# Kernel tuning notes

Measured on AMD Instinct MI355X. Metric: run time of the kernel, lower is better.

Reference implementation:

```python
import jax, jax.numpy as jnp
import numpy as np

# Module config (matches init_kwargs); num_heads must be 1 for the original
# torch code to type-check (score_proj: Linear(d_model, num_heads) applied to
# a head_dim-sized last axis, then squeeze(-1)).
B, S, D, H = 4, 512, 256, 1
DH = D // H  # head_dim == d_model when H == 1


def _linear_init(k, out_f, in_f):
    bound = 1.0 / np.sqrt(in_f)
    kw, kb = jax.random.split(k)
    W = jax.random.uniform(kw, (out_f, in_f), jnp.float32, -bound, bound)
    b = jax.random.uniform(kb, (out_f,), jnp.float32, -bound, bound)
    return W, b


def setup_inputs() -> dict:
    key = jax.random.key(0)
    ks = jax.random.split(key, 8)
    Wq, bq = _linear_init(ks[3], D, D)
    Wk, bk = _linear_init(ks[4], D, D)
    Wv, bv = _linear_init(ks[5], D, D)
    Ws, bs = _linear_init(ks[6], H, D)   # score_proj: d_model -> num_heads
    Wo, bo = _linear_init(ks[7], D, D)
    return {
        "query": jax.random.normal(ks[0], (B, S, D), jnp.float32),
        "key": jax.random.normal(ks[1], (B, S, D), jnp.float32),
        "value": jax.random.normal(ks[2], (B, S, D), jnp.float32),
        "Wq": Wq, "bq": bq, "Wk": Wk, "bk": bk, "Wv": Wv, "bv": bv,
        "Ws": Ws, "bs": bs, "Wo": Wo, "bo": bo,
    }


def reference(query, key, value, Wq, bq, Wk, bk, Wv, bv, Ws, bs, Wo, bo):
    b, s, _ = query.shape
    # Projections, split into heads: (B, H, S, DH)
    q = (query @ Wq.T + bq).reshape(b, s, H, DH).transpose(0, 2, 1, 3)
    k = (key @ Wk.T + bk).reshape(b, s, H, DH).transpose(0, 2, 1, 3)
    v = (value @ Wv.T + bv).reshape(b, s, H, DH).transpose(0, 2, 1, 3)
    # Bahdanau additive scores: tanh of pairwise sum -> (B, H, Sq, Sk, DH)
    t = jnp.tanh(q[:, :, :, None, :] + k[:, :, None, :, :])
    # score_proj (out_features == 1 when H == 1), then squeeze(-1)
    scores = jnp.einsum('bhqkd,od->bhqko', t, Ws) + bs  # (B,H,Sq,Sk,1)
    scores = scores[..., 0]                              # (B,H,Sq,Sk)
    attn = jax.nn.softmax(scores, axis=-1)
    # Weighted sum of values, merge heads back: (B, S, D)
    attended = jnp.einsum('bhqk,bhkd->bqhd', attn, v).reshape(b, s, D)
    out = attended @ Wo.T + bo  # dropout p=0.0 (eval) -> identity
    return out, attn
```

## Files before the change

### kernel.cpp

```cpp
#include <hip/hip_runtime.h>

typedef __attribute__((ext_vector_type(8))) short short8;
typedef __attribute__((ext_vector_type(4))) float f32x4;

constexpr int BATCH = 4;
constexpr int SEQ   = 512;
constexpr int DM    = 256;

#define MFMA(a,b,c) __builtin_amdgcn_mfma_f32_16x16x32_bf16((a),(b),(c),0,0,0)

__device__ __forceinline__ unsigned short bf16h(float x) {
    unsigned u = __float_as_uint(x);
    return (unsigned short)((u + 0x7FFF + ((u >> 16) & 1)) >> 16);
}
__device__ __forceinline__ float bf16f(unsigned short h) {
    return __uint_as_float(((unsigned)h) << 16);
}
__device__ __forceinline__ float exp2x_clamped(float x) {
    x = fminf(5.0f, fmaxf(-5.0f, x));
    return __builtin_amdgcn_exp2f(x * 2.8853900817779268f);
}
__device__ __forceinline__ void cvt8(const float* s, int4& h, int4& l) {
    unsigned hw[8], lw[8];
    #pragma unroll
    for (int j = 0; j < 8; ++j) {
        unsigned short hb = bf16h(s[j]);
        hw[j] = hb;
        lw[j] = bf16h(s[j] - bf16f(hb));
    }
    h.x = (int)(hw[0] | (hw[1] << 16)); h.y = (int)(hw[2] | (hw[3] << 16));
    h.z = (int)(hw[4] | (hw[5] << 16)); h.w = (int)(hw[6] | (hw[7] << 16));
    l.x = (int)(lw[0] | (lw[1] << 16)); l.y = (int)(lw[2] | (lw[3] << 16));
    l.z = (int)(lw[4] | (lw[5] << 16)); l.w = (int)(lw[6] | (lw[7] << 16));
}

template<int EPI, int ASRC, int BSRC>
__device__ __forceinline__ void mfma_core(
    const ushort* __restrict__ Ah, const ushort* __restrict__ Al,
    const float*  __restrict__ A0, const float*  __restrict__ A1, long ldA,
    const ushort* __restrict__ Bh, const ushort* __restrict__ Bl,
    const float*  __restrict__ B0, long ldB,
    float* __restrict__ C, long ldC, const float* __restrict__ bias,
    ushort* __restrict__ Th, ushort* __restrict__ Tl, long ldT)
{
    __shared__ short lds[32768];
    const int tid = threadIdx.x;
    const int i0 = tid, i1 = tid + 256;
    const int r0 = ((i0 >> 7) << 4) | (i0 & 15), r1 = ((i1 >> 7) << 4) | (i1 & 15);
    const int c0 = ((i0 >> 4) & 7) * 8,          c1 = ((i1 >> 4) & 7) * 8;
    const long a0o = (long)r0 * ldA + c0, a1o = (long)r1 * ldA + c1;
    const long b0o = (long)r0 * ldB + c0, b1o = (long)r1 * ldB + c1;

    int4 rah0, rah1, ral0, ral1, rbh0, rbh1, rbl0, rbl1;
    float4 fa00, fa01, fa10, fa11, ga00, ga01, ga10, ga11;
    float4 gb00, gb01, gb10, gb11;

    auto issue_loads = [&](int it) {
        long off = (long)it * 64;
        if constexpr (ASRC != 0) {
            fa00 = *(const float4*)(A0 + a0o + off); fa01 = *(const float4*)(A0 + a0o + off + 4);
            fa10 = *(const float4*)(A0 + a1o + off); fa11 = *(const float4*)(A0 + a1o + off + 4);
            if constexpr (ASRC == 2) {
                ga00 = *(const float4*)(A1 + a0o + off); ga01 = *(const float4*)(A1 + a0o + off + 4);
                ga10 = *(const float4*)(A1 + a1o + off); ga11 = *(const float4*)(A1 + a1o + off + 4);
            }
        } else {
            rah0 = *(const int4*)(Ah + a0o + off); rah1 = *(const int4*)(Ah + a1o + off);
            ral0 = *(const int4*)(Al + a0o + off); ral1 = *(const int4*)(Al + a1o + off);
        }
        if constexpr (BSRC == 1) {
            gb00 = *(const float4*)(B0 + b0o + off); gb01 = *(const float4*)(B0 + b0o + off + 4);
            gb10 = *(const float4*)(B0 + b1o + off); gb11 = *(const float4*)(B0 + b1o + off + 4);
        } else {
            rbh0 = *(const int4*)(Bh + b0o + off); rbh1 = *(const int4*)(Bh + b1o + off);
            rbl0 = *(const int4*)(Bl + b0o + off); rbl1 = *(const int4*)(Bl + b1o + off);
        }
    };
    auto write_lds = [&](int buf) {
        const int bo = buf * 16384;
        if constexpr (ASRC != 0) {
            float s0[8], s1[8];
            if constexpr (ASRC == 2) {
                s0[0]=fa00.x+ga00.x; s0[1]=fa00.y+ga00.y; s0[2]=fa00.z+ga00.z; s0[3]=fa00.w+ga00.w;
                s0[4]=fa01.x+ga01.x; s0[5]=fa01.y+ga01.y; s0[6]=fa01.z+ga01.z; s0[7]=fa01.w+ga01.w;
                s1[0]=fa10.x+ga10.x; s1[1]=fa10.y+ga10.y; s1[2]=fa10.z+ga10.z; s1[3]=fa10.w+ga10.w;
                s1[4]=fa11.x+ga11.x; s1[5]=fa11.y+ga11.y; s1[6]=fa11.z+ga11.z; s1[7]=fa11.w+ga11.w;
            } else {
                s0[0]=fa00.x; s0[1]=fa00.y; s0[2]=fa00.z; s0[3]=fa00.w;
                s0[4]=fa01.x; s0[5]=fa01.y; s0[6]=fa01.z; s0[7]=fa01.w;
                s1[0]=fa10.x; s1[1]=fa10.y; s1[2]=fa10.z; s1[3]=fa10.w;
                s1[4]=fa11.x; s1[5]=fa11.y; s1[6]=fa11.z; s1[7]=fa11.w;
            }
            int4 h, l2;
            cvt8(s0, h, l2);
            *(int4*)&lds[bo + i0 * 8] = h; *(int4*)&lds[bo + 4096 + i0 * 8] = l2;
            cvt8(s1, h, l2);
            *(int4*)&lds[bo + i1 * 8] = h; *(int4*)&lds[bo + 4096 + i1 * 8] = l2;
        } else {
            *(int4*)&lds[bo + i0 * 8] = rah0;        *(int4*)&lds[bo + i1 * 8] = rah1;
            *(int4*)&lds[bo + 4096 + i0 * 8] = ral0; *(int4*)&lds[bo + 4096 + i1 * 8] = ral1;
        }
        if constexpr (BSRC == 1) {
            float s0[8] = {gb00.x, gb00.y, gb00.z, gb00.w, gb01.x, gb01.y, gb01.z, gb01.w};
            float s1[8] = {gb10.x, gb10.y, gb10.z, gb10.w, gb11.x, gb11.y, gb11.z, gb11.w};
            int4 h, l2;
            cvt8(s0, h, l2);
            *(int4*)&lds[bo + 8192 + i0 * 8] = h; *(int4*)&lds[bo + 12288 + i0 * 8] = l2;
            cvt8(s1, h, l2);
            *(int4*)&lds[bo + 8192 + i1 * 8] = h; *(int4*)&lds[bo + 12288 + i1 * 8] = l2;
        } else {
            *(int4*)&lds[bo + 8192  + i0 * 8] = rbh0; *(int4*)&lds[bo + 8192  + i1 * 8] = rbh1;
            *(int4*)&lds[bo + 12288 + i0 * 8] = rbl0; *(int4*)&lds[bo + 12288 + i1 * 8] = rbl1;
        }
    };

    const int l = tid & 63, w = tid >> 6;
    const int ms = (w >> 1) * 2, ns = (w & 1) * 2;
    f32x4 acc00 = {0,0,0,0}, acc01 = {0,0,0,0}, acc10 = {0,0,0,0}, acc11 = {0,0,0,0};

    issue_loads(0);
    write_lds(0);
    __syncthreads();
    for (int it = 0; it < 4; ++it) {
        if (it < 3) issue_loads(it + 1);
        const int bo = (it & 1) * 16384;
        const int lo = l * 8;
        #pragma unroll
        for (int ks = 0; ks < 2; ++ks) {
            short8 a0h = *(const short8*)&lds[bo + ((ms    ) * 2 + ks) * 512 + lo];
            short8 a1h = *(const short8*)&lds[bo + ((ms + 1) * 2 + ks) * 512 + lo];
            short8 a0l = *(const short8*)&lds[bo + 4096 + ((ms    ) * 2 + ks) * 512 + lo];
            short8 a1l = *(const short8*)&lds[bo + 4096 + ((ms + 1) * 2 + ks) * 512 + lo];
            short8 b0h = *(const short8*)&lds[bo + 8192 + ((ns    ) * 2 + ks) * 512 + lo];
            short8 b1h = *(const short8*)&lds[bo + 8192 + ((ns + 1) * 2 + ks) * 512 + lo];
            short8 b0l = *(const short8*)&lds[bo + 12288 + ((ns    ) * 2 + ks) * 512 + lo];
            short8 b1l = *(const short8*)&lds[bo + 12288 + ((ns + 1) * 2 + ks) * 512 + lo];
            acc00 = MFMA(a0h, b0h, acc00); acc00 = MFMA(a0h, b0l, acc00); acc00 = MFMA(a0l, b0h, acc00);
            acc01 = MFMA(a0h, b1h, acc01); acc01 = MFMA(a0h, b1l, acc01); acc01 = MFMA(a0l, b1h, acc01);
            acc10 = MFMA(a1h, b0h, acc10); acc10 = MFMA(a1h, b0l, acc10); acc10 = MFMA(a1l, b0h, acc10);
            acc11 = MFMA(a1h, b1h, acc11); acc11 = MFMA(a1h, b1l, acc11); acc11 = MFMA(a1l, b1h, acc11);
        }
        if (it < 3) {
            write_lds((it + 1) & 1);
            __syncthreads();
        }
    }

    auto epi = [&](int i, int j, f32x4 a) {
        const int n  = (ns + j) * 16 + (l & 15);
        const int mb = (ms + i) * 16 + (l >> 4) * 4;
        if constexpr (EPI == 1) {
            float bb = bias[n];
            float x0 = a.x + bb, x1 = a.y + bb, x2 = a.z + bb, x3 = a.w + bb;
            unsigned short h0 = bf16h(x0), h1 = bf16h(x1), h2 = bf16h(x2), h3 = bf16h(x3);
            int2 ph, pl;
            ph.x = (int)(h0 | ((unsigned)h1 << 16));
            ph.y = (int)(h2 | ((unsigned)h3 << 16));
            pl.x = (int)(bf16h(x0 - bf16f(h0)) | ((unsigned)bf16h(x1 - bf16f(h1)) << 16));
            pl.y = (int)(bf16h(x2 - bf16f(h2)) | ((unsigned)bf16h(x3 - bf16f(h3)) << 16));
            *(int2*)&Th[(long)n * ldT + mb] = ph;
            *(int2*)&Tl[(long)n * ldT + mb] = pl;
        } else {
            float bb = (EPI == 2) ? 0.f : bias[n];
            float xs[4] = {a.x, a.y, a.z, a.w};
            #pragma unroll
            for (int r = 0; r < 4; ++r) {
                float x = xs[r] + bb;
                if constexpr (EPI == 0) x = exp2x_clamped(x);
                C[(long)(mb + r) * ldC + n] = x;
            }
        }
    };
    epi(0, 0, acc00); epi(0, 1, acc01); epi(1, 0, acc10); epi(1, 1, acc11);
}

__global__ __launch_bounds__(256) void proj_mfma(
    const float* __restrict__ q, const float* __restrict__ k, const float* __restrict__ v,
    const float* __restrict__ Wq, const float* __restrict__ Wk, const float* __restrict__ Wv,
    const float* bq, const float* bk, const float* bv,
    float* Eq, float* Ek, ushort* vpTh, ushort* vpTl)
{
    const int z = blockIdx.z;
    const long m0 = blockIdx.x * 64, n0 = blockIdx.y * 64;
    const float* A; const float* B; const float* bias;
    if (z == 0)      { A = q; B = Wq; bias = bq; }
    else if (z == 1) { A = k; B = Wk; bias = bk; }
    else             { A = v; B = Wv; bias = bv; }
    A += m0 * 256; B += n0 * 256; bias += n0;
    if (z < 2) {
        float* C = (z ? Ek : Eq) + m0 * 256 + n0;
        mfma_core<0, 1, 1>(nullptr, nullptr, A, nullptr, 256,
                           nullptr, nullptr, B, 256,
                           C, 256, bias, nullptr, nullptr, 0);
    } else {
        mfma_core<1, 1, 1>(nullptr, nullptr, A, nullptr, 256,
                           nullptr, nullptr, B, 256,
                           nullptr, 0, bias,
                           vpTh + n0 * 2048 + m0, vpTl + n0 * 2048 + m0, 2048);
    }
}

__global__ __launch_bounds__(256) void attnv_mfma(
    const ushort* attn_h, const ushort* attn_l,
    const ushort* vpTh, const ushort* vpTl, float* att0, float* att1)
{
    const int z = blockIdx.z, b = z >> 1, h = z & 1;
    const long m0 = blockIdx.x * 64, n0 = blockIdx.y * 64;
    const long arow = (long)b * SEQ + m0;
    const ushort* Ah = attn_h + arow * SEQ + h * 256;
    const ushort* Al = attn_l + arow * SEQ + h * 256;
    const ushort* Bh = vpTh + n0 * 2048 + (long)b * SEQ + h * 256;
    const ushort* Bl = vpTl + n0 * 2048 + (long)b * SEQ + h * 256;
    float* C = (h ? att1 : att0) + arow * DM + n0;
    mfma_core<2, 0, 0>(Ah, Al, nullptr, nullptr, SEQ,
                       Bh, Bl, nullptr, 2048,
                       C, DM, nullptr, nullptr, nullptr, 0);
}

__global__ __launch_bounds__(256) void out_mfma(
    const float* att0, const float* att1,
    const float* Wo, const float* bo, float* out)
{
    const long m0 = blockIdx.x * 64, n0 = blockIdx.y * 64;
    mfma_core<3, 2, 1>(nullptr, nullptr, att0 + m0 * 256, att1 + m0 * 256, 256,
                       nullptr, nullptr, Wo + n0 * 256, 256,
                       out + m0 * 256 + n0, 256, bo + n0, nullptr, nullptr, 0);
}

__global__ __launch_bounds__(256) void scores_kernel(
    const float* __restrict__ Eq, const float* __restrict__ Ek,
    const float* __restrict__ Ws, float* __restrict__ part)
{
    __shared__ __align__(16) float qL[64][68];
    __shared__ __align__(16) float kL[64][68];
    const int z = blockIdx.z;
    const int b = z >> 1, c = z & 1;
    const int q0 = blockIdx.x * 64, k0 = blockIdx.y * 64;
    const int tid = threadIdx.x;
    const int qi = tid >> 4, ki = tid & 15;

    float acc[4][4] = {};
    for (int cc = 0; cc < 2; ++cc) {
        const int c0 = c * 128 + cc * 64;
        const float* Eqb = Eq + ((long)b * SEQ + q0) * DM + c0;
        const float* Ekb = Ek + ((long)b * SEQ + k0) * DM + c0;
        if (cc) __syncthreads();
        #pragma unroll
        for (int i = 0; i < 4; ++i) {
            int f = i * 256 + tid;
            int r = f >> 4, col = (f & 15) << 2;
            *(float4*)&qL[r][col] = *(const float4*)(Eqb + (long)r * DM + col);
            *(float4*)&kL[r][col] = *(const float4*)(Ekb + (long)r * DM + col);
        }
        __syncthreads();
        #pragma unroll 2
        for (int d = 0; d < 64; d += 4) {
            float4 w4 = *(const float4*)(Ws + c0 + d);
            float4 av[4], bv[4];
            #pragma unroll
            for (int i = 0; i < 4; ++i) av[i] = *(const float4*)&qL[qi + 16 * i][d];
            #pragma unroll
            for (int j = 0; j < 4; ++j) bv[j] = *(const float4*)&kL[ki + 16 * j][d];
            #pragma unroll
            for (int i = 0; i < 4; ++i)
                #pragma unroll
                for (int j = 0; j < 4; ++j) {
                    float xp = fmaf(av[i].x, bv[j].x, 1.0f);
                    float yp = fmaf(av[i].y, bv[j].y, 1.0f);
                    float zp = fmaf(av[i].z, bv[j].z, 1.0f);
                    float wp = fmaf(av[i].w, bv[j].w, 1.0f);
                    float xy = xp * yp, zw = zp * wp;
                    float n1 = fmaf(w4.x, yp, w4.y * xp);
                    float n2 = fmaf(w4.z, wp, w4.w * zp);
                    float num = fmaf(n1, zw, n2 * xy);
                    acc[i][j] = fmaf(num, __builtin_amdgcn_rcpf(xy * zw), acc[i][j]);
                }
        }
    }

    float* pb = part + (long)c * (BATCH * SEQ * SEQ) + (long)b * SEQ * SEQ;
    #pragma unroll
    for (int i = 0; i < 4; ++i) {
        float* row = pb + (long)(q0 + qi + 16 * i) * SEQ + k0 + ki;
        #pragma unroll
        for (int j = 0; j < 4; ++j) row[16 * j] = acc[i][j];
    }
}

__global__ __launch_bounds__(256) void softmax_kernel(
    const float* __restrict__ part, float* __restrict__ attn,
    ushort* __restrict__ attn_h, ushort* __restrict__ attn_l)
{
    __shared__ float red[8];
    const int tid = threadIdx.x;
    const long row = blockIdx.x;
    constexpr long PS = (long)BATCH * SEQ * SEQ;
    const float* p = part + row * SEQ + tid * 2;
    float2 v0 = *(const float2*)(p);
    float2 v1 = *(const float2*)(p + PS);
    float sx = -2.0f * (v0.x + v1.x);
    float sy = -2.0f * (v0.y + v1.y);

    float m = fmaxf(sx, sy);
    #pragma unroll
    for (int off = 32; off; off >>= 1) m = fmaxf(m, __shfl_xor(m, off));
    int wave = tid >> 6;
    if ((tid & 63) == 0) red[wave] = m;
    __syncthreads();
    m = fmaxf(fmaxf(red[0], red[1]), fmaxf(red[2], red[3]));
    constexpr float L2E = 1.4426950408889634f;
    float e0 = __builtin_amdgcn_exp2f((sx - m) * L2E);
    float e1 = __builtin_amdgcn_exp2f((sy - m) * L2E);
    float s = e0 + e1;
    #pragma unroll
    for (int off = 32; off; off >>= 1) s += __shfl_xor(s, off);
    if ((tid & 63) == 0) red[4 + wave] = s;
    __syncthreads();
    float tot = (red[4] + red[5]) + (red[6] + red[7]);
    float inv = __builtin_amdgcn_rcpf(tot);
    float2 o; o.x = e0 * inv; o.y = e1 * inv;
    *(float2*)(attn + row * SEQ + tid * 2) = o;

    unsigned short h0 = bf16h(o.x), h1 = bf16h(o.y);
    unsigned hp = h0 | ((unsigned)h1 << 16);
    unsigned lp = bf16h(o.x - bf16f(h0)) | ((unsigned)bf16h(o.y - bf16f(h1)) << 16);
    *(unsigned*)&attn_h[row * SEQ + tid * 2] = hp;
    *(unsigned*)&attn_l[row * SEQ + tid * 2] = lp;
}

extern "C" void kernel_launch(void* const* d_in, const int* in_sizes, int n_in,
                              void* d_out, int out_size, void* d_ws, size_t ws_size,
                              hipStream_t stream) {
    const float* query = (const float*)d_in[0];
    const float* key   = (const float*)d_in[1];
    const float* value = (const float*)d_in[2];
    const float* Wq = (const float*)d_in[3];
    const float* bq = (const float*)d_in[4];
    const float* Wk = (const float*)d_in[5];
    const float* bk = (const float*)d_in[6];
    const float* Wv = (const float*)d_in[7];
    const float* bv = (const float*)d_in[8];
    const float* Ws = (const float*)d_in[9];
    const float* Wo = (const float*)d_in[11];
    const float* bo = (const float*)d_in[12];

    float* out  = (float*)d_out;
    float* attn = (float*)d_out + (long)BATCH * SEQ * DM;

    float* ws = (float*)d_ws;
    float* Eq   = ws;
    float* Ek   = ws + 524288;
    float* part = ws + 1048576;
    float* att0 = part;
    float* att1 = part + 524288;
    ushort* u = (ushort*)(ws + 1048576 + 2097152);
    ushort* vpTh   = u;              ushort* vpTl   = vpTh + 524288;
    ushort* attn_h = vpTl + 524288;  ushort* attn_l = attn_h + 1048576;

    proj_mfma    <<<dim3(32, 4, 3), 256, 0, stream>>>(query, key, value,
                                                      Wq, Wk, Wv, bq, bk, bv,
                                                      Eq, Ek, vpTh, vpTl);
    scores_kernel<<<dim3(8, 8, 8),  256, 0, stream>>>(Eq, Ek, Ws, part);
    softmax_kernel<<<dim3(2048),    256, 0, stream>>>(part, attn, attn_h, attn_l);
    attnv_mfma   <<<dim3(8, 4, 8),  256, 0, stream>>>(attn_h, attn_l, vpTh, vpTl, att0, att1);
    out_mfma     <<<dim3(32, 4),    256, 0, stream>>>(att0, att1, Wo, bo, out);
}
```

Before: 74.93 us.

## Fuse all stages into one cooperative megakernel with grid syncs and Wo-first reassociation

Replaces the five kernel launches with a single cooperative kernel of 512 blocks that runs projection, scores, softmax and the output stage, separated by grid-wide syncs. The output projection is reassociated so that Wo·V is computed first, alongside the scores, and the final stage does a single attn×(VWo) GEMM with bias, which removes the separate attn·V and out GEMMs. Softmax now assigns one wave per row and drops the max subtraction, relying on bounded scores. The GEMM core also loses its double-buffered LDS pipelining in favour of a single buffer, so global loads overlap compute less, and grid.sync barriers add their own cost.

New measurement: 257.2 us. 3.43x slower.

```diff
diff --git a/kernel.cpp b/kernel.cpp
--- a/kernel.cpp
+++ b/kernel.cpp
@@ -1,4 +1,7 @@
 #include <hip/hip_runtime.h>
+#include <hip/hip_cooperative_groups.h>
+
+namespace cg = cooperative_groups;
 
 typedef __attribute__((ext_vector_type(8))) short short8;
 typedef __attribute__((ext_vector_type(4))) float f32x4;
@@ -37,13 +40,14 @@
 template<int EPI, int ASRC, int BSRC>
 __device__ __forceinline__ void mfma_core(
     const ushort* __restrict__ Ah, const ushort* __restrict__ Al,
-    const float*  __restrict__ A0, const float*  __restrict__ A1, long ldA,
+    const float*  __restrict__ A0, long ldA,
     const ushort* __restrict__ Bh, const ushort* __restrict__ Bl,
     const float*  __restrict__ B0, long ldB,
+    int K,
     float* __restrict__ C, long ldC, const float* __restrict__ bias,
-    ushort* __restrict__ Th, ushort* __restrict__ Tl, long ldT)
+    ushort* __restrict__ Th, ushort* __restrict__ Tl, long ldT,
+    short* lds)
 {
-    __shared__ short lds[32768];
     const int tid = threadIdx.x;
     const int i0 = tid, i1 = tid + 256;
     const int r0 = ((i0 >> 7) << 4) | (i0 & 15), r1 = ((i1 >> 7) << 4) | (i1 & 15);
@@ -52,18 +56,13 @@
     const long b0o = (long)r0 * ldB + c0, b1o = (long)r1 * ldB + c1;
 
     int4 rah0, rah1, ral0, ral1, rbh0, rbh1, rbl0, rbl1;
-    float4 fa00, fa01, fa10, fa11, ga00, ga01, ga10, ga11;
-    float4 gb00, gb01, gb10, gb11;
+    float4 fa00, fa01, fa10, fa11, gb00, gb01, gb10, gb11;
 
     auto issue_loads = [&](int it) {
         long off = (long)it * 64;
-        if constexpr (ASRC != 0) {
+        if constexpr (ASRC == 1) {
             fa00 = *(const float4*)(A0 + a0o + off); fa01 = *(const float4*)(A0 + a0o + off + 4);
             fa10 = *(const float4*)(A0 + a1o + off); fa11 = *(const float4*)(A0 + a1o + off + 4);
-            if constexpr (ASRC == 2) {
-                ga00 = *(const float4*)(A1 + a0o + off); ga01 = *(const float4*)(A1 + a0o + off + 4);
-                ga10 = *(const float4*)(A1 + a1o + off); ga11 = *(const float4*)(A1 + a1o + off + 4);
-            }
         } else {
             rah0 = *(const int4*)(Ah + a0o + off); rah1 = *(const int4*)(Ah + a1o + off);
             ral0 = *(const int4*)(Al + a0o + off); ral1 = *(const int4*)(Al + a1o + off);
@@ -76,41 +75,30 @@
             rbl0 = *(const int4*)(Bl + b0o + off); rbl1 = *(const int4*)(Bl + b1o + off);
         }
     };
-    auto write_lds = [&](int buf) {
-        const int bo = buf * 16384;
-        if constexpr (ASRC != 0) {
-            float s0[8], s1[8];
-            if constexpr (ASRC == 2) {
-                s0[0]=fa00.x+ga00.x; s0[1]=fa00.y+ga00.y; s0[2]=fa00.z+ga00.z; s0[3]=fa00.w+ga00.w;
-                s0[4]=fa01.x+ga01.x; s0[5]=fa01.y+ga01.y; s0[6]=fa01.z+ga01.z; s0[7]=fa01.w+ga01.w;
-                s1[0]=fa10.x+ga10.x; s1[1]=fa10.y+ga10.y; s1[2]=fa10.z+ga10.z; s1[3]=fa10.w+ga10.w;
-                s1[4]=fa11.x+ga11.x; s1[5]=fa11.y+ga11.y; s1[6]=fa11.z+ga11.z; s1[7]=fa11.w+ga11.w;
-            } else {
-                s0[0]=fa00.x; s0[1]=fa00.y; s0[2]=fa00.z; s0[3]=fa00.w;
-                s0[4]=fa01.x; s0[5]=fa01.y; s0[6]=fa01.z; s0[7]=fa01.w;
-                s1[0]=fa10.x; s1[1]=fa10.y; s1[2]=fa10.z; s1[3]=fa10.w;
-                s1[4]=fa11.x; s1[5]=fa11.y; s1[6]=fa11.z; s1[7]=fa11.w;
-            }
+    auto write_lds = [&]() {
+        if constexpr (ASRC == 1) {
+            float s0[8] = {fa00.x, fa00.y, fa00.z, fa00.w, fa01.x, fa01.y, fa01.z, fa01.w};
+            float s1[8] = {fa10.x, fa10.y, fa10.z, fa10.w, fa11.x, fa11.y, fa11.z, fa11.w};
             int4 h, l2;
             cvt8(s0, h, l2);
-            *(int4*)&lds[bo + i0 * 8] = h; *(int4*)&lds[bo + 4096 + i0 * 8] = l2;
+            *(int4*)&lds[i0 * 8] = h; *(int4*)&lds[4096 + i0 * 8] = l2;
             cvt8(s1, h, l2);
-            *(int4*)&lds[bo + i1 * 8] = h; *(int4*)&lds[bo + 4096 + i1 * 8] = l2;
-        } else {
-            *(int4*)&lds[bo + i0 * 8] = rah0;        *(int4*)&lds[bo + i1 * 8] = rah1;
-            *(int4*)&lds[bo + 4096 + i0 * 8] = ral0; *(int4*)&lds[bo + 4096 + i1 * 8] = ral1;
+            *(int4*)&lds[i1 * 8] = h; *(int4*)&lds[4096 + i1 * 8] = l2;
+        } else {
+            *(int4*)&lds[i0 * 8] = rah0;        *(int4*)&lds[i1 * 8] = rah1;
+            *(int4*)&lds[4096 + i0 * 8] = ral0; *(int4*)&lds[4096 + i1 * 8] = ral1;
         }
         if constexpr (BSRC == 1) {
             float s0[8] = {gb00.x, gb00.y, gb00.z, gb00.w, gb01.x, gb01.y, gb01.z, gb01.w};
             float s1[8] = {gb10.x, gb10.y, gb10.z, gb10.w, gb11.x, gb11.y, gb11.z, gb11.w};
             int4 h, l2;
             cvt8(s0, h, l2);
-            *(int4*)&lds[bo + 8192 + i0 * 8] = h; *(int4*)&lds[bo + 12288 + i0 * 8] = l2;
+            *(int4*)&lds[8192 + i0 * 8] = h; *(int4*)&lds[12288 + i0 * 8] = l2;
             cvt8(s1, h, l2);
-            *(int4*)&lds[bo + 8192 + i1 * 8] = h; *(int4*)&lds[bo + 12288 + i1 * 8] = l2;
-        } else {
-            *(int4*)&lds[bo + 8192  + i0 * 8] = rbh0; *(int4*)&lds[bo + 8192  + i1 * 8] = rbh1;
-            *(int4*)&lds[bo + 12288 + i0 * 8] = rbl0; *(int4*)&lds[bo + 12288 + i1 * 8] = rbl1;
+            *(int4*)&lds[8192 + i1 * 8] = h; *(int4*)&lds[12288 + i1 * 8] = l2;
+        } else {
+            *(int4*)&lds[8192  + i0 * 8] = rbh0; *(int4*)&lds[8192  + i1 * 8] = rbh1;
+            *(int4*)&lds[12288 + i0 * 8] = rbl0; *(int4*)&lds[12288 + i1 * 8] = rbl1;
         }
     };
 
@@ -118,50 +106,45 @@
     const int ms = (w >> 1) * 2, ns = (w & 1) * 2;
     f32x4 acc00 = {0,0,0,0}, acc01 = {0,0,0,0}, acc10 = {0,0,0,0}, acc11 = {0,0,0,0};
 
+    const int iters = K >> 6;
     issue_loads(0);
-    write_lds(0);
-    __syncthreads();
-    for (int it = 0; it < 4; ++it) {
-        if (it < 3) issue_loads(it + 1);
-        const int bo = (it & 1) * 16384;
+    for (int it = 0; it < iters; ++it) {
+        write_lds();
+        __syncthreads();
+        if (it + 1 < iters) issue_loads(it + 1);
         const int lo = l * 8;
         #pragma unroll
         for (int ks = 0; ks < 2; ++ks) {
-            short8 a0h = *(const short8*)&lds[bo + ((ms    ) * 2 + ks) * 512 + lo];
-            short8 a1h = *(const short8*)&lds[bo + ((ms + 1) * 2 + ks) * 512 + lo];
-            short8 a0l = *(const short8*)&lds[bo + 4096 + ((ms    ) * 2 + ks) * 512 + lo];
-            short8 a1l = *(const short8*)&lds[bo + 4096 + ((ms + 1) * 2 + ks) * 512 + lo];
-            short8 b0h = *(const short8*)&lds[bo + 8192 + ((ns    ) * 2 + ks) * 512 + lo];
-            short8 b1h = *(const short8*)&lds[bo + 8192 + ((ns + 1) * 2 + ks) * 512 + lo];
-            short8 b0l = *(const short8*)&lds[bo + 12288 + ((ns    ) * 2 + ks) * 512 + lo];
-            short8 b1l = *(const short8*)&lds[bo + 12288 + ((ns + 1) * 2 + ks) * 512 + lo];
+            short8 a0h = *(const short8*)&lds[((ms    ) * 2 + ks) * 512 + lo];
+            short8 a1h = *(const short8*)&lds[((ms + 1) * 2 + ks) * 512 + lo];
+            short8 a0l = *(const short8*)&lds[4096 + ((ms    ) * 2 + ks) * 512 + lo];
+            short8 a1l = *(const short8*)&lds[4096 + ((ms + 1) * 2 + ks) * 512 + lo];
+            short8 b0h = *(const short8*)&lds[8192 + ((ns    ) * 2 + ks) * 512 + lo];
+            short8 b1h = *(const short8*)&lds[8192 + ((ns + 1) * 2 + ks) * 512 + lo];
+            short8 b0l = *(const short8*)&lds[12288 + ((ns    ) * 2 + ks) * 512 + lo];
+            short8 b1l = *(const short8*)&lds[12288 + ((ns + 1) * 2 + ks) * 512 + lo];
             acc00 = MFMA(a0h, b0h, acc00); acc00 = MFMA(a0h, b0l, acc00); acc00 = MFMA(a0l, b0h, acc00);
             acc01 = MFMA(a0h, b1h, acc01); acc01 = MFMA(a0h, b1l, acc01); acc01 = MFMA(a0l, b1h, acc01);
             acc10 = MFMA(a1h, b0h, acc10); acc10 = MFMA(a1h, b0l, acc10); acc10 = MFMA(a1l, b0h, acc10);
             acc11 = MFMA(a1h, b1h, acc11); acc11 = MFMA(a1h, b1l, acc11); acc11 = MFMA(a1l, b1h, acc11);
         }
-        if (it < 3) {
-            write_lds((it + 1) & 1);
-            __syncthreads();
-        }
+        __syncthreads();
     }
 
     auto epi = [&](int i, int j, f32x4 a) {
         const int n  = (ns + j) * 16 + (l & 15);
         const int mb = (ms + i) * 16 + (l >> 4) * 4;
         if constexpr (EPI == 1) {
+            float bb = bias ? bias[n] : 0.0f;
+            float xs[4] = {a.x + bb, a.y + bb, a.z + bb, a.w + bb};
+            #pragma unroll
+            for (int r = 0; r < 4; ++r) {
+                unsigned short h = bf16h(xs[r]);
+                Th[(long)(mb + r) * ldT + n] = h;
+                Tl[(long)(mb + r) * ldT + n] = bf16h(xs[r] - bf16f(h));
+            }
+        } else {
             float bb = bias[n];
-            float x0 = a.x + bb, x1 = a.y + bb, x2 = a.z + bb, x3 = a.w + bb;
-            unsigned short h0 = bf16h(x0), h1 = bf16h(x1), h2 = bf16h(x2), h3 = bf16h(x3);
-            int2 ph, pl;
-            ph.x = (int)(h0 | ((unsigned)h1 << 16));
-            ph.y = (int)(h2 | ((unsigned)h3 << 16));
-            pl.x = (int)(bf16h(x0 - bf16f(h0)) | ((unsigned)bf16h(x1 - bf16f(h1)) << 16));
-            pl.y = (int)(bf16h(x2 - bf16f(h2)) | ((unsigned)bf16h(x3 - bf16f(h3)) << 16));
-            *(int2*)&Th[(long)n * ldT + mb] = ph;
-            *(int2*)&Tl[(long)n * ldT + mb] = pl;
-        } else {
-            float bb = (EPI == 2) ? 0.f : bias[n];
             float xs[4] = {a.x, a.y, a.z, a.w};
             #pragma unroll
             for (int r = 0; r < 4; ++r) {
@@ -174,68 +157,14 @@
     epi(0, 0, acc00); epi(0, 1, acc01); epi(1, 0, acc10); epi(1, 1, acc11);
 }
 
-__global__ __launch_bounds__(256) void proj_mfma(
-    const float* __restrict__ q, const float* __restrict__ k, const float* __restrict__ v,
-    const float* __restrict__ Wq, const float* __restrict__ Wk, const float* __restrict__ Wv,
-    const float* bq, const float* bk, const float* bv,
-    float* Eq, float* Ek, ushort* vpTh, ushort* vpTl)
-{
-    const int z = blockIdx.z;
-    const long m0 = blockIdx.x * 64, n0 = blockIdx.y * 64;
-    const float* A; const float* B; const float* bias;
-    if (z == 0)      { A = q; B = Wq; bias = bq; }
-    else if (z == 1) { A = k; B = Wk; bias = bk; }
-    else             { A = v; B = Wv; bias = bv; }
-    A += m0 * 256; B += n0 * 256; bias += n0;
-    if (z < 2) {
-        float* C = (z ? Ek : Eq) + m0 * 256 + n0;
-        mfma_core<0, 1, 1>(nullptr, nullptr, A, nullptr, 256,
-                           nullptr, nullptr, B, 256,
-                           C, 256, bias, nullptr, nullptr, 0);
-    } else {
-        mfma_core<1, 1, 1>(nullptr, nullptr, A, nullptr, 256,
-                           nullptr, nullptr, B, 256,
-                           nullptr, 0, bias,
-                           vpTh + n0 * 2048 + m0, vpTl + n0 * 2048 + m0, 2048);
-    }
-}
-
-__global__ __launch_bounds__(256) void attnv_mfma(
-    const ushort* attn_h, const ushort* attn_l,
-    const ushort* vpTh, const ushort* vpTl, float* att0, float* att1)
-{
-    const int z = blockIdx.z, b = z >> 1, h = z & 1;
-    const long m0 = blockIdx.x * 64, n0 = blockIdx.y * 64;
-    const long arow = (long)b * SEQ + m0;
-    const ushort* Ah = attn_h + arow * SEQ + h * 256;
-    const ushort* Al = attn_l + arow * SEQ + h * 256;
-    const ushort* Bh = vpTh + n0 * 2048 + (long)b * SEQ + h * 256;
-    const ushort* Bl = vpTl + n0 * 2048 + (long)b * SEQ + h * 256;
-    float* C = (h ? att1 : att0) + arow * DM + n0;
-    mfma_core<2, 0, 0>(Ah, Al, nullptr, nullptr, SEQ,
-                       Bh, Bl, nullptr, 2048,
-                       C, DM, nullptr, nullptr, nullptr, 0);
-}
-
-__global__ __launch_bounds__(256) void out_mfma(
-    const float* att0, const float* att1,
-    const float* Wo, const float* bo, float* out)
-{
-    const long m0 = blockIdx.x * 64, n0 = blockIdx.y * 64;
-    mfma_core<3, 2, 1>(nullptr, nullptr, att0 + m0 * 256, att1 + m0 * 256, 256,
-                       nullptr, nullptr, Wo + n0 * 256, 256,
-                       out + m0 * 256 + n0, 256, bo + n0, nullptr, nullptr, 0);
-}
-
-__global__ __launch_bounds__(256) void scores_kernel(
-    const float* __restrict__ Eq, const float* __restrict__ Ek,
+__device__ __forceinline__ void scores_job(
+    int j, float* sm, const float* __restrict__ Eq, const float* __restrict__ Ek,
     const float* __restrict__ Ws, float* __restrict__ part)
 {
-    __shared__ __align__(16) float qL[64][68];
-    __shared__ __align__(16) float kL[64][68];
-    const int z = blockIdx.z;
-    const int b = z >> 1, c = z & 1;
-    const int q0 = blockIdx.x * 64, k0 = blockIdx.y * 64;
+    float (*qL)[68] = (float (*)[68])sm;
+    float (*kL)[68] = (float (*)[68])(sm + 64 * 68);
+    const int qx = j & 7, ky = (j >> 3) & 7, b = (j >> 6) & 3, c = j >> 8;
+    const int q0 = qx * 64, k0 = ky * 64;
     const int tid = threadIdx.x;
     const int qi = tid >> 4, ki = tid & 15;
 
@@ -260,20 +189,20 @@
             #pragma unroll
             for (int i = 0; i < 4; ++i) av[i] = *(const float4*)&qL[qi + 16 * i][d];
             #pragma unroll
-            for (int j = 0; j < 4; ++j) bv[j] = *(const float4*)&kL[ki + 16 * j][d];
+            for (int jj = 0; jj < 4; ++jj) bv[jj] = *(const float4*)&kL[ki + 16 * jj][d];
             #pragma unroll
             for (int i = 0; i < 4; ++i)
                 #pragma unroll
-                for (int j = 0; j < 4; ++j) {
-                    float xp = fmaf(av[i].x, bv[j].x, 1.0f);
-                    float yp = fmaf(av[i].y, bv[j].y, 1.0f);
-                    float zp = fmaf(av[i].z, bv[j].z, 1.0f);
-                    float wp = fmaf(av[i].w, bv[j].w, 1.0f);
+                for (int jj = 0; jj < 4; ++jj) {
+                    float xp = fmaf(av[i].x, bv[jj].x, 1.0f);
+                    float yp = fmaf(av[i].y, bv[jj].y, 1.0f);
+                    float zp = fmaf(av[i].z, bv[jj].z, 1.0f);
+                    float wp = fmaf(av[i].w, bv[jj].w, 1.0f);
                     float xy = xp * yp, zw = zp * wp;
                     float n1 = fmaf(w4.x, yp, w4.y * xp);
                     float n2 = fmaf(w4.z, wp, w4.w * zp);
                     float num = fmaf(n1, zw, n2 * xy);
-                    acc[i][j] = fmaf(num, __builtin_amdgcn_rcpf(xy * zw), acc[i][j]);
+                    acc[i][jj] = fmaf(num, __builtin_amdgcn_rcpf(xy * zw), acc[i][jj]);
                 }
         }
     }
@@ -283,85 +212,143 @@
     for (int i = 0; i < 4; ++i) {
         float* row = pb + (long)(q0 + qi + 16 * i) * SEQ + k0 + ki;
         #pragma unroll
-        for (int j = 0; j < 4; ++j) row[16 * j] = acc[i][j];
-    }
-}
-
-__global__ __launch_bounds__(256) void softmax_kernel(
-    const float* __restrict__ part, float* __restrict__ attn,
-    ushort* __restrict__ attn_h, ushort* __restrict__ attn_l)
+        for (int jj = 0; jj < 4; ++jj) row[16 * jj] = acc[i][jj];
+    }
+}
+
+struct MegaArgs {
+    const float *q, *k, *v, *Wq, *bq, *Wk, *bk, *Wv, *bv, *Ws, *Wo, *bo;
+    float *out, *attn, *Eq, *Ek, *part;
+    ushort *vph, *vpl, *pvoTh, *pvoTl, *ah, *al;
+};
+
+__global__ __launch_bounds__(256, 2) void mega(MegaArgs A)
 {
-    __shared__ float red[8];
+    __shared__ __align__(16) char smem[34816];
+    short* lds = (short*)smem;
+    cg::grid_group grid = cg::this_grid();
+    const int bid = blockIdx.x;
     const int tid = threadIdx.x;
-    const long row = blockIdx.x;
-    constexpr long PS = (long)BATCH * SEQ * SEQ;
-    const float* p = part + row * SEQ + tid * 2;
-    float2 v0 = *(const float2*)(p);
-    float2 v1 = *(const float2*)(p + PS);
-    float sx = -2.0f * (v0.x + v1.x);
-    float sy = -2.0f * (v0.y + v1.y);
-
-    float m = fmaxf(sx, sy);
-    #pragma unroll
-    for (int off = 32; off; off >>= 1) m = fmaxf(m, __shfl_xor(m, off));
-    int wave = tid >> 6;
-    if ((tid & 63) == 0) red[wave] = m;
-    __syncthreads();
-    m = fmaxf(fmaxf(red[0], red[1]), fmaxf(red[2], red[3]));
-    constexpr float L2E = 1.4426950408889634f;
-    float e0 = __builtin_amdgcn_exp2f((sx - m) * L2E);
-    float e1 = __builtin_amdgcn_exp2f((sy - m) * L2E);
-    float s = e0 + e1;
-    #pragma unroll
-    for (int off = 32; off; off >>= 1) s += __shfl_xor(s, off);
-    if ((tid & 63) == 0) red[4 + wave] = s;
-    __syncthreads();
-    float tot = (red[4] + red[5]) + (red[6] + red[7]);
-    float inv = __builtin_amdgcn_rcpf(tot);
-    float2 o; o.x = e0 * inv; o.y = e1 * inv;
-    *(float2*)(attn + row * SEQ + tid * 2) = o;
-
-    unsigned short h0 = bf16h(o.x), h1 = bf16h(o.y);
-    unsigned hp = h0 | ((unsigned)h1 << 16);
-    unsigned lp = bf16h(o.x - bf16f(h0)) | ((unsigned)bf16h(o.y - bf16f(h1)) << 16);
-    *(unsigned*)&attn_h[row * SEQ + tid * 2] = hp;
-    *(unsigned*)&attn_l[row * SEQ + tid * 2] = lp;
+
+    if (bid < 384) {
+        const int z = bid >> 7, t = bid & 127;
+        const long m0 = (long)(t >> 2) * 64, n0 = (long)(t & 3) * 64;
+        const float* Ain = (z == 0) ? A.q : (z == 1) ? A.k : A.v;
+        const float* W   = (z == 0) ? A.Wq : (z == 1) ? A.Wk : A.Wv;
+        const float* bs  = (z == 0) ? A.bq : (z == 1) ? A.bk : A.bv;
+        if (z < 2) {
+            float* C = z ? A.Ek : A.Eq;
+            mfma_core<0, 1, 1>(nullptr, nullptr, Ain + m0 * 256, 256,
+                               nullptr, nullptr, W + n0 * 256, 256, 256,
+                               C + m0 * 256 + n0, 256, bs + n0,
+                               nullptr, nullptr, 0, lds);
+        } else {
+            mfma_core<1, 1, 1>(nullptr, nullptr, Ain + m0 * 256, 256,
+                               nullptr, nullptr, W + n0 * 256, 256, 256,
+                               nullptr, 0, bs + n0,
+                               A.vph + m0 * 256 + n0, A.vpl + m0 * 256 + n0, 256, lds);
+        }
+    }
+    grid.sync();
+
+    scores_job(bid, (float*)smem, A.Eq, A.Ek, A.Ws, A.part);
+    if ((bid & 3) == 0) {
+        __syncthreads();
+        const int j = bid >> 2;
+        const int b = j >> 5, t = j & 31;
+        const long m0 = (long)(t >> 3) * 64;
+        const long n0 = (long)(t & 7) * 64;
+        mfma_core<1, 1, 0>(nullptr, nullptr, A.Wo + m0 * 256, 256,
+                           A.vph + ((long)b * SEQ + n0) * 256,
+                           A.vpl + ((long)b * SEQ + n0) * 256, nullptr, 256, 256,
+                           nullptr, 0, nullptr,
+                           A.pvoTh + ((long)b * 256 + m0) * 512 + n0,
+                           A.pvoTl + ((long)b * 256 + m0) * 512 + n0, 512, lds);
+    }
+    grid.sync();
+
+    {
+        const int wv = tid >> 6, ln = tid & 63;
+        const long row = (long)bid * 4 + wv;
+        const float* p0 = A.part + row * SEQ + ln * 4;
+        const float* p1 = p0 + (long)BATCH * SEQ * SEQ;
+        float4 a0 = *(const float4*)p0;
+        float4 a1 = *(const float4*)(p0 + 256);
+        float4 b0 = *(const float4*)p1;
+        float4 b1 = *(const float4*)(p1 + 256);
+        constexpr float NL2E = -2.0f * 1.4426950408889634f;
+        float e0 = __builtin_amdgcn_exp2f(NL2E * (a0.x + b0.x));
+        float e1 = __builtin_amdgcn_exp2f(NL2E * (a0.y + b0.y));
+        float e2 = __builtin_amdgcn_exp2f(NL2E * (a0.z + b0.z));
+        float e3 = __builtin_amdgcn_exp2f(NL2E * (a0.w + b0.w));
+        float e4 = __builtin_amdgcn_exp2f(NL2E * (a1.x + b1.x));
+        float e5 = __builtin_amdgcn_exp2f(NL2E * (a1.y + b1.y));
+        float e6 = __builtin_amdgcn_exp2f(NL2E * (a1.z + b1.z));
+        float e7 = __builtin_amdgcn_exp2f(NL2E * (a1.w + b1.w));
+        float s = ((e0 + e1) + (e2 + e3)) + ((e4 + e5) + (e6 + e7));
+        #pragma unroll
+        for (int off = 32; off; off >>= 1) s += __shfl_xor(s, off);
+        float inv = __builtin_amdgcn_rcpf(s);
+        float4 o0 = {e0 * inv, e1 * inv, e2 * inv, e3 * inv};
+        float4 o1 = {e4 * inv, e5 * inv, e6 * inv, e7 * inv};
+        *(float4*)(A.attn + row * SEQ + ln * 4) = o0;
+        *(float4*)(A.attn + row * SEQ + 256 + ln * 4) = o1;
+        unsigned short h0 = bf16h(o0.x), h1 = bf16h(o0.y), h2 = bf16h(o0.z), h3 = bf16h(o0.w);
+        unsigned short g0 = bf16h(o1.x), g1 = bf16h(o1.y), g2 = bf16h(o1.z), g3 = bf16h(o1.w);
+        uint2 hp0 = {h0 | ((unsigned)h1 << 16), h2 | ((unsigned)h3 << 16)};
+        uint2 hp1 = {g0 | ((unsigned)g1 << 16), g2 | ((unsigned)g3 << 16)};
+        uint2 lp0 = {bf16h(o0.x - bf16f(h0)) | ((unsigned)bf16h(o0.y - bf16f(h1)) << 16),
+                     bf16h(o0.z - bf16f(h2)) | ((unsigned)bf16h(o0.w - bf16f(h3)) << 16)};
+        uint2 lp1 = {bf16h(o1.x - bf16f(g0)) | ((unsigned)bf16h(o1.y - bf16f(g1)) << 16),
+                     bf16h(o1.z - bf16f(g2)) | ((unsigned)bf16h(o1.w - bf16f(g3)) << 16)};
+        *(uint2*)&A.ah[row * SEQ + ln * 4] = hp0;
+        *(uint2*)&A.ah[row * SEQ + 256 + ln * 4] = hp1;
+        *(uint2*)&A.al[row * SEQ + ln * 4] = lp0;
+        *(uint2*)&A.al[row * SEQ + 256 + ln * 4] = lp1;
+    }
+    grid.sync();
+
+    if ((bid & 3) == 1) {
+        const int j = bid >> 2;
+        const int b = j >> 5, t = j & 31;
+        const long mt = t >> 2, nt = t & 3;
+        const long arow = (long)b * SEQ + mt * 64;
+        mfma_core<2, 0, 0>(A.ah + arow * 512, A.al + arow * 512, nullptr, 512,
+                           A.pvoTh + ((long)b * 256 + nt * 64) * 512,
+                           A.pvoTl + ((long)b * 256 + nt * 64) * 512, nullptr, 512, 512,
+                           A.out + arow * 256 + nt * 64, 256, A.bo + nt * 64,
+                           nullptr, nullptr, 0, lds);
+    }
 }
 
 extern "C" void kernel_launch(void* const* d_in, const int* in_sizes, int n_in,
                               void* d_out, int out_size, void* d_ws, size_t ws_size,
                               hipStream_t stream) {
-    const float* query = (const float*)d_in[0];
-    const float* key   = (const float*)d_in[1];
-    const float* value = (const float*)d_in[2];
-    const float* Wq = (const float*)d_in[3];
-    const float* bq = (const float*)d_in[4];
-    const float* Wk = (const float*)d_in[5];
-    const float* bk = (const float*)d_in[6];
-    const float* Wv = (const float*)d_in[7];
-    const float* bv = (const float*)d_in[8];
-    const float* Ws = (const float*)d_in[9];
-    const float* Wo = (const float*)d_in[11];
-    const float* bo = (const float*)d_in[12];
-
-    float* out  = (float*)d_out;
-    float* attn = (float*)d_out + (long)BATCH * SEQ * DM;
-
     float* ws = (float*)d_ws;
     float* Eq   = ws;
     float* Ek   = ws + 524288;
     float* part = ws + 1048576;
-    float* att0 = part;
-    float* att1 = part + 524288;
     ushort* u = (ushort*)(ws + 1048576 + 2097152);
-    ushort* vpTh   = u;              ushort* vpTl   = vpTh + 524288;
-    ushort* attn_h = vpTl + 524288;  ushort* attn_l = attn_h + 1048576;
-
-    proj_mfma    <<<dim3(32, 4, 3), 256, 0, stream>>>(query, key, value,
-                                                      Wq, Wk, Wv, bq, bk, bv,
-                                                      Eq, Ek, vpTh, vpTl);
-    scores_kernel<<<dim3(8, 8, 8),  256, 0, stream>>>(Eq, Ek, Ws, part);
-    softmax_kernel<<<dim3(2048),    256, 0, stream>>>(part, attn, attn_h, attn_l);
-    attnv_mfma   <<<dim3(8, 4, 8),  256, 0, stream>>>(attn_h, attn_l, vpTh, vpTl, att0, att1);
-    out_mfma     <<<dim3(32, 4),    256, 0, stream>>>(att0, att1, Wo, bo, out);
-}
+    ushort* vph   = u;                ushort* vpl   = vph + 524288;
+    ushort* pvoTh = vpl + 524288;     ushort* pvoTl = pvoTh + 524288;
+    ushort* ah    = pvoTl + 524288;   ushort* al    = ah + 1048576;
+
+    MegaArgs a;
+    a.q  = (const float*)d_in[0];
+    a.k  = (const float*)d_in[1];
+    a.v  = (const float*)d_in[2];
+    a.Wq = (const float*)d_in[3];  a.bq = (const float*)d_in[4];
+    a.Wk = (const float*)d_in[5];  a.bk = (const float*)d_in[6];
+    a.Wv = (const float*)d_in[7];  a.bv = (const float*)d_in[8];
+    a.Ws = (const float*)d_in[9];
+    a.Wo = (const float*)d_in[11]; a.bo = (const float*)d_in[12];
+    a.out  = (float*)d_out;
+    a.attn = (float*)d_out + (long)BATCH * SEQ * DM;
+    a.Eq = Eq; a.Ek = Ek; a.part = part;
+    a.vph = vph; a.vpl = vpl; a.pvoTh = pvoTh; a.pvoTl = pvoTl;
+    a.ah = ah; a.al = al;
+
+    void* params[1] = { &a };
+    hipLaunchCooperativeKernel((const void*)mega, dim3(512), dim3(256),
+                               params, 0, stream);
+}
```
